# Kernel optimization log

Measured on AMD Instinct MI355X. Metric: run time of the kernel, lower is better.

## Reference

```python
import jax, jax.numpy as jnp
import numpy as np

# module hyper-params (from NLSearch __init__ defaults)
K = 7        # top-k neighbors
PS = 7       # patch size
WS = 8       # search window (ws x ws candidates)
NHEADS = 1
STRIDE0 = 4  # query grid stride
STRIDE1 = 1  # candidate stride within window


def _reflect(i, n):
    # reflect (mirror) out-of-range indices into [0, n)
    i = jnp.where(i < 0, -i, i)
    return jnp.where(i >= n, 2 * (n - 1) - i, i)


def setup_inputs() -> dict:
    key = jax.random.key(0)
    k0, k1 = jax.random.split(key)
    vid0 = jax.random.normal(k0, (1, 3, 32, 256, 256), dtype=jnp.float32)
    vid1 = jax.random.normal(k1, (1, 3, 32, 256, 256), dtype=jnp.float32)
    return {"vid0": vid0, "vid1": vid1}


def _nl_search(vid0, vid1):
    B, T, C, H, W = vid0.shape
    HD = NHEADS
    c = C // HD
    v0 = vid0.reshape(B, T, HD, c, H, W)
    v1 = vid1.reshape(B, T, HD, c, H, W)
    nH = (H - 1) // STRIDE0 + 1
    nW = (W - 1) // STRIDE0 + 1
    qh = jnp.arange(nH) * STRIDE0  # query centers
    qw = jnp.arange(nW) * STRIDE0
    poff = jnp.arange(PS) - PS // 2  # centered patch offsets

    def patches(v, hc, wc):
        # gather reflect-bounded ps x ps patches centered at (hc, wc)
        hi = _reflect(hc[:, None] + poff[None, :], H)  # [nH, PS]
        wi = _reflect(wc[:, None] + poff[None, :], W)  # [nW, PS]
        p = v[:, :, :, :, hi]          # [B,T,HD,c,nH,PS,W]
        p = p[:, :, :, :, :, :, wi]    # [B,T,HD,c,nH,PS,nW,PS]
        return p

    p0 = patches(v0, qh, qw)  # query patches, reused across all shifts
    woff = (jnp.arange(WS) - WS // 2) * STRIDE1
    shifts = jnp.stack(jnp.meshgrid(woff, woff, indexing='ij'), -1).reshape(-1, 2)  # [WS*WS,2]

    def body(carry, s):
        def step(s_):
            p1 = patches(v1, qh + s_[0], qw + s_[1])
            # patch inner product ('prod' search distance)
            return jnp.einsum('bthcnivj,bthcnivj->bthnv', p0, p1)
        return carry, jax.checkpoint(step)(s)

    _, dists = jax.lax.scan(body, 0, shifts)   # [L,B,T,HD,nH,nW]
    dists = jnp.moveaxis(dists, 0, -1)         # [B,T,HD,nH,nW,L]

    # anchor_self: force the self (zero-shift) candidate to rank first,
    # but return its true distance (bump only used for ordering)
    self_idx = (WS // 2) * WS + (WS // 2)
    adj = dists.at[..., self_idx].add(jnp.asarray(1e30, dists.dtype))
    _, top_idx = jax.lax.top_k(adj, K)                       # [B,T,HD,nH,nW,K]
    top_d = jnp.take_along_axis(dists, top_idx, axis=-1)     # [B,T,HD,nH,nW,K]

    # decode flat shift index -> absolute (t,h,w) neighbor coordinates
    dh = (top_idx // WS - WS // 2) * STRIDE1
    dw = (top_idx % WS - WS // 2) * STRIDE1
    hh = _reflect(qh[None, None, None, :, None, None] + dh, H)
    ww = _reflect(qw[None, None, None, None, :, None] + dw, W)
    tt = jnp.broadcast_to(jnp.arange(T)[None, :, None, None, None, None], hh.shape)
    inds = jnp.stack([tt, hh, ww], -1)  # [B,T,HD,nH,nW,K,3]

    Q = T * nH * nW
    dists_out = jnp.transpose(top_d, (0, 2, 1, 3, 4, 5)).reshape(B, HD, Q, K)
    inds_out = jnp.transpose(inds, (0, 2, 1, 3, 4, 5, 6)).reshape(B, HD, Q, K, 3)
    return dists_out, inds_out


def reference(vid0, vid1):
    return _nl_search(vid0, vid1)
```

## Files before the change

### kernel.cpp

```cpp
#include <hip/hip_runtime.h>

#define TT 3
#define CCH 32
#define HH 256
#define WW 256
#define KK 7
#define NQ 64
#define QPB 16
#define V1W 76
#define V1R 14
#define V1N (V1R*V1W)
#define V1P 1088
#define CHC 8
#define NCHUNK 4

__device__ __forceinline__ int refl(int i, int n) {
    i = i < 0 ? -i : i;
    return i >= n ? 2*(n-1) - i : i;
}

__device__ __forceinline__ void gload_lds(const float* g, float* l) {
    __builtin_amdgcn_global_load_lds(
        (const __attribute__((address_space(1))) unsigned int*)g,
        (__attribute__((address_space(3))) unsigned int*)l, 4, 0, 0);
}

#define FMABLOCK(RR)                                                     \
    _Pragma("unroll")                                                    \
    for (int a = 0; a < 4; ++a) {                                        \
        const int pi = (RR) - a;                                         \
        if (pi >= 0 && pi < 7) {                                         \
            _Pragma("unroll")                                            \
            for (int sw = 0; sw < 8; ++sw)                               \
                _Pragma("unroll")                                        \
                for (int j = 0; j < 7; ++j)                              \
                    acc[a][sw] += x[pi][j] * y[sw + j];                  \
        }                                                                \
    }

#define ROW(RR, C0,C1,C2v,C3v, N0,N1,N2,N3)                              \
    {                                                                    \
        if ((RR) + 1 < 10) {                                             \
            const float4* yp = (const float4*)(ybase + (4*shh + (RR) + 1) * V1W); \
            N0 = yp[0]; N1 = yp[1]; N2 = yp[2]; N3 = yp[3];              \
        }                                                                \
        const float y[16] = {C0.x,C0.y,C0.z,C0.w,  C1.x,C1.y,C1.z,C1.w,  \
                             C2v.x,C2v.y,C2v.z,C2v.w, C3v.x,C3v.y,C3v.z,C3v.w}; \
        FMABLOCK(RR)                                                     \
    }

__global__ __launch_bounds__(256, 3)
void nls_kernel(const float* __restrict__ vid0, const float* __restrict__ vid1,
                float* __restrict__ out) {
    __shared__ float v1s[CHC * V1P];

    const int bx  = blockIdx.x;
    const int t   = bx >> 8;
    const int rem = bx & 255;
    const int qy  = rem >> 2;
    const int q0  = (rem & 3) * QPB;
    const int qh  = qy * 4;
    const int w0  = 4*q0 - 7;

    const int tid   = threadIdx.x;
    const int qwi   = tid & 15;
    const int c01   = (tid >> 4) & 3;
    const int c2    = (tid >> 6) & 1;
    const int shh   = tid >> 7;
    const int clane = c01 + 4*c2;
    const int qx    = q0 + qwi;

    int off1[5];
#pragma unroll
    for (int k = 0; k < 5; ++k) {
        int idx = tid + 256*k;
        if (idx < V1N) {
            int r = idx / V1W, wi = idx - r*V1W;
            off1[k] = refl(qh + r - 7, HH) * WW + refl(w0 + wi, WW);
        } else off1[k] = 0;
    }

    float acc[4][8];
#pragma unroll
    for (int a = 0; a < 4; ++a)
#pragma unroll
        for (int b = 0; b < 8; ++b) acc[a][b] = 0.f;

    const float* g0t = vid0 + (size_t)t * (CCH*HH*WW);
    const float* g1t = vid1 + (size_t)t * (CCH*HH*WW);

#pragma unroll 1
    for (int s = 0; s < NCHUNK; ++s) {
        __syncthreads();
#pragma unroll
        for (int ch = 0; ch < CHC; ++ch) {
            const float* p1 = g1t + (size_t)(CHC*s + ch) * (HH*WW);
            float* lb = &v1s[ch*V1P + (tid & ~63)];
#pragma unroll
            for (int k = 0; k < 4; ++k)
                gload_lds(p1 + off1[k], lb + 256*k);
            if (tid < V1N - 1024)
                gload_lds(p1 + off1[4], &v1s[ch*V1P + 1024 + (tid & ~63)]);
        }

        const float* p0 = g0t + (size_t)(CHC*s + clane) * (HH*WW);
        float x[7][8];
#pragma unroll
        for (int i = 0; i < 7; ++i) {
            const float* rowp = p0 + refl(qh + i - 3, HH) * WW;
            float4 B = *(const float4*)(rowp + 4*qx);
            float4 A;
            if (qx > 0) A = *(const float4*)(rowp + 4*qx - 4);
            else        A = make_float4(0.f, B.w, B.z, B.y);
            x[i][0]=A.y; x[i][1]=A.z; x[i][2]=A.w;
            x[i][3]=B.x; x[i][4]=B.y; x[i][5]=B.z; x[i][6]=B.w;
        }
        __syncthreads();

        const float* ybase = &v1s[clane*V1P + 4*qwi];
        float4 Ya0, Ya1, Ya2, Ya3, Yb0, Yb1, Yb2, Yb3;
        {
            const float4* yp = (const float4*)(ybase + (4*shh) * V1W);
            Ya0 = yp[0]; Ya1 = yp[1]; Ya2 = yp[2]; Ya3 = yp[3];
        }
        ROW(0, Ya0,Ya1,Ya2,Ya3, Yb0,Yb1,Yb2,Yb3)
        ROW(1, Yb0,Yb1,Yb2,Yb3, Ya0,Ya1,Ya2,Ya3)
        ROW(2, Ya0,Ya1,Ya2,Ya3, Yb0,Yb1,Yb2,Yb3)
        ROW(3, Yb0,Yb1,Yb2,Yb3, Ya0,Ya1,Ya2,Ya3)
        ROW(4, Ya0,Ya1,Ya2,Ya3, Yb0,Yb1,Yb2,Yb3)
        ROW(5, Yb0,Yb1,Yb2,Yb3, Ya0,Ya1,Ya2,Ya3)
        ROW(6, Ya0,Ya1,Ya2,Ya3, Yb0,Yb1,Yb2,Yb3)
        ROW(7, Yb0,Yb1,Yb2,Yb3, Ya0,Ya1,Ya2,Ya3)
        ROW(8, Ya0,Ya1,Ya2,Ya3, Yb0,Yb1,Yb2,Yb3)
        ROW(9, Yb0,Yb1,Yb2,Yb3, Ya0,Ya1,Ya2,Ya3)
    }

#pragma unroll
    for (int m = 16; m <= 32; m <<= 1)
#pragma unroll
        for (int a = 0; a < 4; ++a)
#pragma unroll
            for (int b = 0; b < 8; ++b)
                acc[a][b] += __shfl_xor(acc[a][b], m, 64);

    __syncthreads();
    float* dlds = v1s;
    if (c01 == 0) {
#pragma unroll
        for (int a = 0; a < 4; ++a) {
            float* dp = &dlds[c2*1024 + qwi*64 + (shh*4 + a)*8];
            *(float4*)(dp)     = make_float4(acc[a][0], acc[a][1], acc[a][2], acc[a][3]);
            *(float4*)(dp + 4) = make_float4(acc[a][4], acc[a][5], acc[a][6], acc[a][7]);
        }
    }
    __syncthreads();

    {
        const int q16 = tid >> 4;
        const int l16 = tid & 15;
        const float* d0 = &dlds[q16 * 64];
        const float* d1 = d0 + 1024;
        const int j0 = l16 * 4;
        float cv[4];
#pragma unroll
        for (int jj = 0; jj < 4; ++jj) {
            float v = d0[j0 + jj] + d1[j0 + jj];
            if (j0 + jj == 36) v += 1e30f;
            cv[jj] = v;
        }
        unsigned mask = 0;
        const int qxx = q0 + q16;
        const int q   = (t*NQ + qy)*NQ + qxx;
        float* od = out + q*KK;
        float* oi = out + (size_t)TT*NQ*NQ*KK + (size_t)q*KK*3;
        for (int k = 0; k < KK; ++k) {
            float best = -3.4e38f; int bi = 1 << 30;
#pragma unroll
            for (int jj = 0; jj < 4; ++jj)
                if (!(mask & (1u << jj)) && cv[jj] > best) { best = cv[jj]; bi = j0 + jj; }
#pragma unroll
            for (int m = 1; m <= 8; m <<= 1) {
                float ob = __shfl_xor(best, m, 64);
                int  obi = __shfl_xor(bi,  m, 64);
                if (ob > best || (ob == best && obi < bi)) { best = ob; bi = obi; }
            }
            if ((bi >> 2) == l16) mask |= 1u << (bi & 3);
            if (l16 == 0) {
                od[k] = d0[bi] + d1[bi];
                int dh = (bi >> 3) - 4;
                int dw = (bi & 7) - 4;
                oi[k*3 + 0] = (float)t;
                oi[k*3 + 1] = (float)refl(qh + dh, HH);
                oi[k*3 + 2] = (float)refl(qxx*4 + dw, WW);
            }
        }
    }
}

extern "C" void kernel_launch(void* const* d_in, const int* in_sizes, int n_in,
                              void* d_out, int out_size, void* d_ws, size_t ws_size,
                              hipStream_t stream) {
    (void)in_sizes; (void)n_in; (void)d_ws; (void)ws_size; (void)out_size;
    const float* vid0 = (const float*)d_in[0];
    const float* vid1 = (const float*)d_in[1];
    float* out = (float*)d_out;
    nls_kernel<<<dim3(TT * NQ * (NQ / QPB)), dim3(256), 0, stream>>>(vid0, vid1, out);
}
```

Measured before the change: 123.9 us.

## Split channel reduction across two blocks and move top-k into second kernel

The fused kernel is split into a partial-dot-product kernel, where each block handles half of the 32 channels (twice as many blocks), and a separate top-k kernel that sums the two partial distance maps from workspace and selects the neighbors. Launch bounds rise from 3 to 4 blocks per CU. The aim is more parallelism and occupancy on a grid that previously had only 768 blocks. The cost is an extra kernel launch plus a workspace write and read of the partial distances.

```diff
diff --git a/kernel.cpp b/kernel.cpp
--- a/kernel.cpp
+++ b/kernel.cpp
@@ -12,7 +12,7 @@
 #define V1N (V1R*V1W)
 #define V1P 1088
 #define CHC 8
-#define NCHUNK 4
+#define NCHUNK 2
 
 __device__ __forceinline__ int refl(int i, int n) {
     i = i < 0 ? -i : i;
@@ -49,18 +49,20 @@
         FMABLOCK(RR)                                                     \
     }
 
-__global__ __launch_bounds__(256, 3)
-void nls_kernel(const float* __restrict__ vid0, const float* __restrict__ vid1,
-                float* __restrict__ out) {
+__global__ __launch_bounds__(256, 4)
+void nls_partial(const float* __restrict__ vid0, const float* __restrict__ vid1,
+                 float* __restrict__ ws) {
     __shared__ float v1s[CHC * V1P];
 
-    const int bx  = blockIdx.x;
-    const int t   = bx >> 8;
-    const int rem = bx & 255;
-    const int qy  = rem >> 2;
-    const int q0  = (rem & 3) * QPB;
-    const int qh  = qy * 4;
-    const int w0  = 4*q0 - 7;
+    const int bx   = blockIdx.x;
+    const int half = bx & 1;
+    const int b2   = bx >> 1;
+    const int t    = b2 >> 8;
+    const int rem  = b2 & 255;
+    const int qy   = rem >> 2;
+    const int q0   = (rem & 3) * QPB;
+    const int qh   = qy * 4;
+    const int w0   = 4*q0 - 7;
 
     const int tid   = threadIdx.x;
     const int qwi   = tid & 15;
@@ -86,8 +88,8 @@
 #pragma unroll
         for (int b = 0; b < 8; ++b) acc[a][b] = 0.f;
 
-    const float* g0t = vid0 + (size_t)t * (CCH*HH*WW);
-    const float* g1t = vid1 + (size_t)t * (CCH*HH*WW);
+    const float* g0t = vid0 + ((size_t)t*CCH + half*16) * (HH*WW);
+    const float* g1t = vid1 + ((size_t)t*CCH + half*16) * (HH*WW);
 
 #pragma unroll 1
     for (int s = 0; s < NCHUNK; ++s) {
@@ -156,43 +158,63 @@
     __syncthreads();
 
     {
-        const int q16 = tid >> 4;
-        const int l16 = tid & 15;
-        const float* d0 = &dlds[q16 * 64];
-        const float* d1 = d0 + 1024;
-        const int j0 = l16 * 4;
-        float cv[4];
-#pragma unroll
-        for (int jj = 0; jj < 4; ++jj) {
-            float v = d0[j0 + jj] + d1[j0 + jj];
-            if (j0 + jj == 36) v += 1e30f;
-            cv[jj] = v;
-        }
-        unsigned mask = 0;
-        const int qxx = q0 + q16;
-        const int q   = (t*NQ + qy)*NQ + qxx;
-        float* od = out + q*KK;
-        float* oi = out + (size_t)TT*NQ*NQ*KK + (size_t)q*KK*3;
-        for (int k = 0; k < KK; ++k) {
-            float best = -3.4e38f; int bi = 1 << 30;
-#pragma unroll
-            for (int jj = 0; jj < 4; ++jj)
-                if (!(mask & (1u << jj)) && cv[jj] > best) { best = cv[jj]; bi = j0 + jj; }
-#pragma unroll
-            for (int m = 1; m <= 8; m <<= 1) {
-                float ob = __shfl_xor(best, m, 64);
-                int  obi = __shfl_xor(bi,  m, 64);
-                if (ob > best || (ob == best && obi < bi)) { best = ob; bi = obi; }
-            }
-            if ((bi >> 2) == l16) mask |= 1u << (bi & 3);
-            if (l16 == 0) {
-                od[k] = d0[bi] + d1[bi];
-                int dh = (bi >> 3) - 4;
-                int dw = (bi & 7) - 4;
-                oi[k*3 + 0] = (float)t;
-                oi[k*3 + 1] = (float)refl(qh + dh, HH);
-                oi[k*3 + 2] = (float)refl(qxx*4 + dw, WW);
-            }
+        float4 A = *(const float4*)&dlds[4*tid];
+        float4 B = *(const float4*)&dlds[1024 + 4*tid];
+        float4 R = make_float4(A.x+B.x, A.y+B.y, A.z+B.z, A.w+B.w);
+        *(float4*)(ws + (size_t)bx*1024 + 4*tid) = R;
+    }
+}
+
+__global__ __launch_bounds__(256, 4)
+void nls_topk(const float* __restrict__ ws, float* __restrict__ out) {
+    __shared__ float dlds[QPB * 64];
+    const int p   = blockIdx.x;
+    const int t   = p >> 8;
+    const int rem = p & 255;
+    const int qy  = rem >> 2;
+    const int q0  = (rem & 3) * QPB;
+    const int qh  = qy * 4;
+    const int tid = threadIdx.x;
+
+    const float* a = ws + (size_t)p * 2048;
+    for (int i = tid; i < 1024; i += 256) dlds[i] = a[i] + a[i + 1024];
+    __syncthreads();
+
+    const int q16 = tid >> 4;
+    const int l16 = tid & 15;
+    const float* d = &dlds[q16 * 64];
+    const int j0 = l16 * 4;
+    float cv[4];
+#pragma unroll
+    for (int jj = 0; jj < 4; ++jj) {
+        float v = d[j0 + jj];
+        if (j0 + jj == 36) v += 1e30f;
+        cv[jj] = v;
+    }
+    unsigned mask = 0;
+    const int qx = q0 + q16;
+    const int q  = (t*NQ + qy)*NQ + qx;
+    float* od = out + q*KK;
+    float* oi = out + (size_t)TT*NQ*NQ*KK + (size_t)q*KK*3;
+    for (int k = 0; k < KK; ++k) {
+        float best = -3.4e38f; int bi = 1 << 30;
+#pragma unroll
+        for (int jj = 0; jj < 4; ++jj)
+            if (!(mask & (1u << jj)) && cv[jj] > best) { best = cv[jj]; bi = j0 + jj; }
+#pragma unroll
+        for (int m = 1; m <= 8; m <<= 1) {
+            float ob = __shfl_xor(best, m, 64);
+            int  obi = __shfl_xor(bi,  m, 64);
+            if (ob > best || (ob == best && obi < bi)) { best = ob; bi = obi; }
+        }
+        if ((bi >> 2) == l16) mask |= 1u << (bi & 3);
+        if (l16 == 0) {
+            od[k] = d[bi];
+            int dh = (bi >> 3) - 4;
+            int dw = (bi & 7) - 4;
+            oi[k*3 + 0] = (float)t;
+            oi[k*3 + 1] = (float)refl(qh + dh, HH);
+            oi[k*3 + 2] = (float)refl(qx*4 + dw, WW);
         }
     }
 }
@@ -200,9 +222,11 @@
 extern "C" void kernel_launch(void* const* d_in, const int* in_sizes, int n_in,
                               void* d_out, int out_size, void* d_ws, size_t ws_size,
                               hipStream_t stream) {
-    (void)in_sizes; (void)n_in; (void)d_ws; (void)ws_size; (void)out_size;
+    (void)in_sizes; (void)n_in; (void)ws_size; (void)out_size;
     const float* vid0 = (const float*)d_in[0];
     const float* vid1 = (const float*)d_in[1];
     float* out = (float*)d_out;
-    nls_kernel<<<dim3(TT * NQ * (NQ / QPB)), dim3(256), 0, stream>>>(vid0, vid1, out);
-}
+    float* ws  = (float*)d_ws;
+    nls_partial<<<dim3(2 * TT * NQ * (NQ / QPB)), dim3(256), 0, stream>>>(vid0, vid1, ws);
+    nls_topk<<<dim3(TT * NQ * (NQ / QPB)), dim3(256), 0, stream>>>(ws, out);
+}
```

New measurement: 193.2 us. 1.56x slower.
